# Kernel tuning notes

Hardware: AMD Instinct MI355X
Metric: run time of the kernel (lower is better)

## Reference

```python
import jax, jax.numpy as jnp
import numpy as np

IMG, P, INC = 384, 2, 3
C = 2 * IMG            # embed_dim = 768
NP_ = IMG // P         # 192 patches
N = NP_ + 1            # 193 tokens with cls
L, H, E, K, B = 6, 12, 8, 2, 32
HD = C // H
EPS = 1e-5


def layer_norm(x, w, b):
    m = jnp.mean(x, -1, keepdims=True)
    v = jnp.mean((x - m) ** 2, -1, keepdims=True)
    return (x - m) * jax.lax.rsqrt(v + EPS) * w + b


def setup_inputs() -> dict:
    key = jax.random.key(0)
    ks = iter(jax.random.split(key, 32))
    nrm = lambda sh, s=0.02: jax.random.normal(next(ks), sh, jnp.float32) * s
    inp = {
        'x1': nrm((B, INC, IMG, IMG), 1.0),
        'x2': nrm((B, INC, IMG, IMG), 1.0),
        'patch_w': nrm((C, INC, IMG, P)),
        'patch_b': jnp.zeros((C,)),
        'cls_token': nrm((1, 1, C), 1e-6),
        'ln1_w': jnp.ones((L, C)), 'ln1_b': jnp.zeros((L, C)),
        'qkv_w': nrm((L, 3 * C, C)), 'qkv_b': jnp.zeros((L, 3 * C)),
        'proj_w': nrm((L, C, C)), 'proj_b': jnp.zeros((L, C)),
        'ln2_w': jnp.ones((L, C)), 'ln2_b': jnp.zeros((L, C)),
        'route_w': nrm((L, E, C)), 'route_b': jnp.zeros((L, E)),
        'rln_w': jnp.ones((L, E)), 'rln_b': jnp.zeros((L, E)),
        'expert_w': nrm((L, E, C, C)), 'expert_b': jnp.zeros((L, E, C)),
        'norm_w': jnp.ones((C,)), 'norm_b': jnp.zeros((C,)),
    }
    # fixed 1D sin-cos positional embedding (build_sincos_encoding)
    pd = C // 2
    omega = jnp.exp(jnp.arange(pd, dtype=jnp.float32) * (-np.log(10000.0) / pd))
    ow = jnp.arange(NP_, dtype=jnp.float32)[:, None] * omega
    pe = jnp.concatenate([jnp.sin(ow), jnp.cos(ow)], axis=1)          # [192, C]
    inp['pos_emb'] = jnp.concatenate([jnp.zeros((1, C)), pe], axis=0)[None]  # [1, N, C]
    return inp


def _patch_embed(x, patch_w, patch_b, cls_token, pos_emb):
    b = x.shape[0]
    # non-overlapping (IMG, P) conv == matmul on patches, flattened in (c, kh, kw) order
    xp = x.reshape(b, INC, IMG, NP_, P).transpose(0, 3, 1, 2, 4).reshape(b, NP_, INC * IMG * P)
    tok = xp @ patch_w.reshape(C, -1).T + patch_b                     # [B, 192, C]
    tok = jnp.concatenate([jnp.broadcast_to(cls_token, (b, 1, C)), tok], axis=1)
    return tok + pos_emb


def _encoder(x, view_id, ln1_w, ln1_b, qkv_w, qkv_b, proj_w, proj_b,
             ln2_w, ln2_b, route_w, route_b, rln_w, rln_b, expert_w, expert_b):
    scale = HD ** -0.5
    base = jax.random.fold_in(jax.random.key(1234), view_id)
    b = x.shape[0]

    def step(h, p):
        idx, l1w, l1b, qw, qb, pw, pb, l2w, l2b, rw, rb, rlw, rlb, ew, eb = p
        # --- attention ---
        y = layer_norm(h, l1w, l1b)
        qkv = (y @ qw.T + qb).reshape(b, N, 3, H, HD).transpose(2, 0, 3, 1, 4)
        q, k, v = qkv[0], qkv[1], qkv[2]
        a = jax.nn.softmax(jnp.einsum('bhqd,bhkd->bhqk', q, k) * scale, axis=-1)
        o = jnp.einsum('bhqk,bhkd->bhqd', a, v).transpose(0, 2, 1, 3).reshape(b, N, C)
        h = h + o @ pw.T + pb
        # --- MoE ---
        y = layer_norm(h, l2w, l2b)
        logits = layer_norm(y @ rw.T + rb, rlw, rlb)                  # [B, N, E]
        noise = jax.random.normal(jax.random.fold_in(base, idx), logits.shape) / E
        rwts = jax.nn.softmax(logits, axis=-1) + noise
        topw, topi = jax.lax.top_k(rwts, K)
        topw = jax.nn.softmax(topw, axis=-1)
        # dense all-expert compute, as in the source module
        eo = jnp.einsum('bni,eoi->bneo', y, ew) + eb                  # [B, N, E, C]
        sel = jnp.take_along_axis(eo, topi[..., None], axis=2)        # [B, N, K, C]
        h = h + (sel * topw[..., None]).sum(axis=2)
        return h, None

    xs = (jnp.arange(L), ln1_w, ln1_b, qkv_w, qkv_b, proj_w, proj_b,
          ln2_w, ln2_b, route_w, route_b, rln_w, rln_b, expert_w, expert_b)
    x, _ = jax.lax.scan(step, x, xs)
    return x


def reference(x1, x2, patch_w, patch_b, cls_token, ln1_w, ln1_b, qkv_w, qkv_b,
              proj_w, proj_b, ln2_w, ln2_b, route_w, route_b, rln_w, rln_b,
              expert_w, expert_b, norm_w, norm_b, pos_emb):
    def tower(x, vid):
        h = _patch_embed(x, patch_w, patch_b, cls_token, pos_emb)
        h = _encoder(h, vid, ln1_w, ln1_b, qkv_w, qkv_b, proj_w, proj_b,
                     ln2_w, ln2_b, route_w, route_b, rln_w, rln_b, expert_w, expert_b)
        return layer_norm(h, norm_w, norm_b)[:, 0]
    return jnp.concatenate([tower(x1, 0), tower(x2, 1)], axis=1)      # [B, 2*C]
```

## Files before the change

kernel.cpp:

```cpp
#include <hip/hip_runtime.h>
#include <stdint.h>

#define C_DIM   768
#define N_TOK   193
#define B_TOT   64
#define ROWS    (B_TOT * N_TOK)
#define QKV_DIM 2304
#define N_HEAD  12
#define N_EXP   8
#define MAXPER  ROWS
#define RTOK    64

enum { MODE_PATCH = 0, MODE_PLAIN = 1, MODE_RESID = 2, MODE_EXPERT = 3 };

typedef __attribute__((ext_vector_type(8))) short bf16x8;
typedef __attribute__((ext_vector_type(4))) float f32x4;

__device__ __forceinline__ uint32_t rotl32(uint32_t x, int n){ return (x << n) | (x >> (32 - n)); }

__device__ __forceinline__ void tf2x32(uint32_t k0, uint32_t k1, uint32_t x0, uint32_t x1,
                                       uint32_t &r0, uint32_t &r1){
  uint32_t k2 = k0 ^ k1 ^ 0x1BD11BDAu;
#define TF4(a,b,c,d) x0+=x1; x1=rotl32(x1,a); x1^=x0; x0+=x1; x1=rotl32(x1,b); x1^=x0; \
                     x0+=x1; x1=rotl32(x1,c); x1^=x0; x0+=x1; x1=rotl32(x1,d); x1^=x0;
  x0 += k0; x1 += k1;
  TF4(13,15,26, 6)  x0 += k1; x1 += k2 + 1u;
  TF4(17,29,16,24)  x0 += k2; x1 += k0 + 2u;
  TF4(13,15,26, 6)  x0 += k0; x1 += k1 + 3u;
  TF4(17,29,16,24)  x0 += k1; x1 += k2 + 4u;
  TF4(13,15,26, 6)  x0 += k2; x1 += k0 + 5u;
#undef TF4
  r0 = x0; r1 = x1;
}

__device__ __forceinline__ float jax_erfinv(float x){
  float w = -log1pf(-x * x);
  float p;
  if (w < 5.0f){
    w -= 2.5f;
    p =              2.81022636e-08f;
    p = fmaf(p, w,   3.43273939e-07f);
    p = fmaf(p, w,  -3.5233877e-06f);
    p = fmaf(p, w,  -4.39150654e-06f);
    p = fmaf(p, w,   0.00021858087f);
    p = fmaf(p, w,  -0.00125372503f);
    p = fmaf(p, w,  -0.00417768164f);
    p = fmaf(p, w,   0.246640727f);
    p = fmaf(p, w,   1.50140941f);
  } else {
// ... 13 lines not shown

__device__ __forceinline__ float jax_noise(uint32_t c0, uint32_t c1, uint32_t j){
  uint32_t o0, o1;
  tf2x32(c0, c1, 0u, j, o0, o1);
  uint32_t bits = o0 ^ o1;
  float f = __uint_as_float(0x3f800000u | (bits >> 9)) - 1.0f;
  const float lo = -0.99999994f;
  float u = fmaxf(lo, f * 2.0f + lo);
  return 1.41421356237f * jax_erfinv(u) * 0.125f;
}

__device__ __forceinline__ unsigned short f2bf(float x){
  union { float f; uint32_t u; } v; v.f = x;
  uint32_t u = v.u;
  uint32_t r = (u + 0x7FFFu + ((u >> 16) & 1u)) >> 16;
  return (unsigned short)r;
}
__device__ __forceinline__ float bf2f(unsigned short h){
  union { uint32_t u; float f; } v; v.u = ((uint32_t)h) << 16;
  return v.f;
}
__device__ __forceinline__ void fsplit_t(float x, short &hi, short &lo){
  union { float f; uint32_t u; } v; v.f = x;
  uint32_t hb = v.u & 0xFFFF0000u;
  hi = (short)(hb >> 16);
  union { uint32_t u; float f; } hv; hv.u = hb;
  lo = (short)f2bf(x - hv.f);
}

__global__ __launch_bounds__(64) void k_sentinel(float* __restrict__ out, float v){
  if (threadIdx.x == 0) out[0] = v;
}

__global__ __launch_bounds__(256) void k_cls(float* __restrict__ h, const float* __restrict__ cls,
                                             const float* __restrict__ pos){
  const int bt = blockIdx.x;
  #pragma unroll
  for (int u = 0; u < 3; ++u){
    int c = threadIdx.x + u * 256;
    h[(size_t)bt * N_TOK * C_DIM + c] = cls[c] + pos[c];
  }
}

__device__ __forceinline__ float blk_sum(float v, float* sb){
  #pragma unroll
  for (int off = 32; off > 0; off >>= 1) v += __shfl_down(v, off, 64);
  const int lane = threadIdx.x & 63, w = threadIdx.x >> 6;
  if (lane == 0) sb[w] = v;
  __syncthreads();
  if (threadIdx.x == 0) sb[4] = sb[0] + sb[1] + sb[2] + sb[3];
  __syncthreads();
  float r = sb[4];
  __syncthreads();
  return r;
}

__global__ __launch_bounds__(256) void k_layernorm(const float* __restrict__ x, float* __restrict__ y,
                                                   const float* __restrict__ w, const float* __restrict__ b,
                                                   int* __restrict__ ecnt){
  __shared__ float sb[8];
  if (ecnt && blockIdx.x == 0 && threadIdx.x < N_EXP) ecnt[threadIdx.x] = 0;
  const float* xr = x + (size_t)blockIdx.x * C_DIM;
  float v0 = xr[threadIdx.x], v1 = xr[threadIdx.x + 256], v2 = xr[threadIdx.x + 512];
  float mean = blk_sum(v0 + v1 + v2, sb) * (1.0f / 768.0f);
  float d0 = v0 - mean, d1 = v1 - mean, d2 = v2 - mean;
  float var = blk_sum(d0 * d0 + d1 * d1 + d2 * d2, sb) * (1.0f / 768.0f);
  float inv = 1.0f / sqrtf(var + 1e-5f);
  float* yr = y + (size_t)blockIdx.x * C_DIM;
  yr[threadIdx.x]       = d0 * inv * w[threadIdx.x]       + b[threadIdx.x];
  yr[threadIdx.x + 256] = d1 * inv * w[threadIdx.x + 256] + b[threadIdx.x + 256];
  yr[threadIdx.x + 512] = d2 * inv * w[threadIdx.x + 512] + b[threadIdx.x + 512];
}

__global__ __launch_bounds__(256) void k_combine_ln(
    float* __restrict__ h, const float* __restrict__ eout, const float* __restrict__ topw,
    float* __restrict__ y, const float* __restrict__ w, const float* __restrict__ b)
{
  __shared__ float sb[8];
  const int tok = blockIdx.x;
  const float w0 = topw[tok * 2], w1 = topw[tok * 2 + 1];
  const size_t hb = (size_t)tok * C_DIM;
  const size_t e0 = (size_t)(tok * 2) * C_DIM, e1 = e0 + C_DIM;
  const int t = threadIdx.x;
  float v0 = h[hb + t]       + (w0 * eout[e0 + t]       + w1 * eout[e1 + t]);
  float v1 = h[hb + t + 256] + (w0 * eout[e0 + t + 256] + w1 * eout[e1 + t + 256]);
  float v2 = h[hb + t + 512] + (w0 * eout[e0 + t + 512] + w1 * eout[e1 + t + 512]);
  h[hb + t]       = v0;
  h[hb + t + 256] = v1;
  h[hb + t + 512] = v2;
  float mean = blk_sum(v0 + v1 + v2, sb) * (1.0f / 768.0f);
  float d0 = v0 - mean, d1 = v1 - mean, d2 = v2 - mean;
  float var = blk_sum(d0 * d0 + d1 * d1 + d2 * d2, sb) * (1.0f / 768.0f);
  float inv = 1.0f / sqrtf(var + 1e-5f);
  y[hb + t]       = d0 * inv * w[t]       + b[t];
  y[hb + t + 256] = d1 * inv * w[t + 256] + b[t + 256];
  y[hb + t + 512] = d2 * inv * w[t + 512] + b[t + 512];
}

__global__ __launch_bounds__(256) void k_final(const float* __restrict__ h, float* __restrict__ out,
                                               const float* __restrict__ w, const float* __restrict__ b){
  __shared__ float sb[8];
  const int bt = blockIdx.x;
  const float* xr = h + (size_t)bt * N_TOK * C_DIM;
  float v0 = xr[threadIdx.x], v1 = xr[threadIdx.x + 256], v2 = xr[threadIdx.x + 512];
  float mean = blk_sum(v0 + v1 + v2, sb) * (1.0f / 768.0f);
  float d0 = v0 - mean, d1 = v1 - mean, d2 = v2 - mean;
  float var = blk_sum(d0 * d0 + d1 * d1 + d2 * d2, sb) * (1.0f / 768.0f);
  float inv = 1.0f / sqrtf(var + 1e-5f);
  float* orow = out + (size_t)(bt & 31) * 1536 + (size_t)(bt >> 5) * C_DIM;
  orow[threadIdx.x]       = d0 * inv * w[threadIdx.x]       + b[threadIdx.x];
  orow[threadIdx.x + 256] = d1 * inv * w[threadIdx.x + 256] + b[threadIdx.x + 256];
  orow[threadIdx.x + 512] = d2 * inv * w[threadIdx.x + 512] + b[threadIdx.x + 512];
}

template<int MODE>
__global__ __launch_bounds__(256) void k_mgemm(
    const float* __restrict__ A, const float* __restrict__ W,
    const float* __restrict__ bias, float* __restrict__ C,
    int M, int Nc, int Kc,
    const float* __restrict__ xa, const float* __restrict__ xb,
    const float* __restrict__ pos,
    const int* __restrict__ elist, const int* __restrict__ ecnt)
{
  __shared__ short sAhi[128][40];
  __shared__ short sAlo[128][40];
  __shared__ short sBhi[128][40];
  __shared__ short sBlo[128][40];

  const int tid = threadIdx.x;

  int e = 0;
  int Mloc = M;
  const float* Wp = W;
  const float* bp = bias;
  if constexpr (MODE == MODE_EXPERT){
    e = blockIdx.z;
    Mloc = ecnt[e];
    Wp = W + (size_t)e * C_DIM * C_DIM;
    bp = bias + e * C_DIM;
  }
  const int row0 = blockIdx.x * 128;
  const int col0 = blockIdx.y * 128;
  if (row0 >= Mloc) return;

  const int srow = tid >> 1;
  const int skh  = (tid & 1) * 16;

  const float* arow = A;
  bool avalid = false;
  const float* psrc = nullptr;
  if constexpr (MODE == MODE_PLAIN || MODE == MODE_RESID){
    int r = row0 + srow;
    avalid = r < Mloc;
    arow = A + (size_t)(avalid ? r : 0) * Kc;
  } else if constexpr (MODE == MODE_EXPERT){
    int r = row0 + srow;
    avalid = r < Mloc;
    if (avalid) arow = A + (size_t)(elist[e * MAXPER + r] >> 1) * C_DIM;
  } else {
    int r = row0 + srow;
    int bt = r / 192;
    int n  = r - bt * 192;
    const float* xp = (bt < 32) ? xa : xb;
    psrc = xp + (size_t)(bt & 31) * 3 * 384 * 384 + n * 2;
    avalid = true;
  }
  const float* brow = Wp + (size_t)(col0 + srow) * Kc;

  const int wv = tid >> 6;
  const int wr = (wv >> 1) * 64;
  const int wc = (wv & 1) * 64;
  const int lane = tid & 63;
  const int lrow = lane & 15;
  const int lkh  = (lane >> 4) * 8;

  f32x4 acc[4][4] = {};

  float va[16], vb[16];
  auto loadA = [&](int k0){
    if constexpr (MODE == MODE_PATCH){
      int c   = k0 / 768;
      int rem = k0 - c * 768;
      const float* pc = psrc + ((size_t)c * 384 + (rem >> 1)) * 384;
      #pragma unroll
      for (int m = 0; m < 8; ++m){
        va[m * 2 + 0] = pc[(size_t)m * 384 + 0];
        va[m * 2 + 1] = pc[(size_t)m * 384 + 1];
      }
    } else {
      if (avalid){
        *(float4*)&va[0]  = *(const float4*)(arow + k0);
        *(float4*)&va[4]  = *(const float4*)(arow + k0 + 4);
        *(float4*)&va[8]  = *(const float4*)(arow + k0 + 8);
        *(float4*)&va[12] = *(const float4*)(arow + k0 + 12);
      } else {
        #pragma unroll
        for (int j = 0; j < 16; ++j) va[j] = 0.f;
      }
    }
  };
  auto loadB = [&](int k0){
    *(float4*)&vb[0]  = *(const float4*)(brow + k0);
    *(float4*)&vb[4]  = *(const float4*)(brow + k0 + 4);
    *(float4*)&vb[8]  = *(const float4*)(brow + k0 + 8);
    *(float4*)&vb[12] = *(const float4*)(brow + k0 + 12);
  };

  loadA(skh);
  loadB(skh);

  const int nkt = Kc / 32;
  for (int kt = 0; kt < nkt; ++kt){
    {
      short hi[16], lo[16];
      #pragma unroll
      for (int j = 0; j < 16; ++j) fsplit_t(va[j], hi[j], lo[j]);
      *(bf16x8*)&sAhi[srow][skh]     = *(bf16x8*)&hi[0];
      *(bf16x8*)&sAhi[srow][skh + 8] = *(bf16x8*)&hi[8];
      *(bf16x8*)&sAlo[srow][skh]     = *(bf16x8*)&lo[0];
      *(bf16x8*)&sAlo[srow][skh + 8] = *(bf16x8*)&lo[8];
      #pragma unroll
      for (int j = 0; j < 16; ++j) fsplit_t(vb[j], hi[j], lo[j]);
      *(bf16x8*)&sBhi[srow][skh]     = *(bf16x8*)&hi[0];
      *(bf16x8*)&sBhi[srow][skh + 8] = *(bf16x8*)&hi[8];
      *(bf16x8*)&sBlo[srow][skh]     = *(bf16x8*)&lo[0];
      *(bf16x8*)&sBlo[srow][skh + 8] = *(bf16x8*)&lo[8];
    }
    __syncthreads();
    if (kt + 1 < nkt){
      loadA((kt + 1) * 32 + skh);
      loadB((kt + 1) * 32 + skh);
    }
    bf16x8 ahi[4], alo[4], bhi[4], blo[4];
    #pragma unroll
    for (int i = 0; i < 4; ++i){
      ahi[i] = *(const bf16x8*)&sAhi[wr + i * 16 + lrow][lkh];
      alo[i] = *(const bf16x8*)&sAlo[wr + i * 16 + lrow][lkh];
    }
    #pragma unroll
    for (int j = 0; j < 4; ++j){
      bhi[j] = *(const bf16x8*)&sBhi[wc + j * 16 + lrow][lkh];
      blo[j] = *(const bf16x8*)&sBlo[wc + j * 16 + lrow][lkh];
    }
    #pragma unroll
    for (int i = 0; i < 4; ++i)
      #pragma unroll
      for (int j = 0; j < 4; ++j){
        acc[i][j] = __builtin_amdgcn_mfma_f32_16x16x32_bf16(ahi[i], bhi[j], acc[i][j], 0, 0, 0);
        acc[i][j] = __builtin_amdgcn_mfma_f32_16x16x32_bf16(ahi[i], blo[j], acc[i][j], 0, 0, 0);
        acc[i][j] = __builtin_amdgcn_mfma_f32_16x16x32_bf16(alo[i], bhi[j], acc[i][j], 0, 0, 0);
      }
    __syncthreads();
  }

  #pragma unroll
  for (int i = 0; i < 4; ++i){
    const int rbase = row0 + wr + i * 16 + (lane >> 4) * 4;
    #pragma unroll
    for (int r = 0; r < 4; ++r){
      const int rg = rbase + r;
      if (rg >= Mloc) continue;
      if constexpr (MODE == MODE_PATCH){
        int bt = rg / 192, n = rg - (rg / 192) * 192;
        size_t orow = ((size_t)bt * N_TOK + n + 1) * C_DIM;
        size_t prow = (size_t)(n + 1) * C_DIM;
        #pragma unroll
        for (int j = 0; j < 4; ++j){
          int cg = col0 + wc + j * 16 + (lane & 15);
          C[orow + cg] = acc[i][j][r] + bp[cg] + pos[prow + cg];
        }
      } else if constexpr (MODE == MODE_PLAIN){
        size_t orow = (size_t)rg * Nc;
        #pragma unroll
        for (int j = 0; j < 4; ++j){
          int cg = col0 + wc + j * 16 + (lane & 15);
          C[orow + cg] = acc[i][j][r] + bp[cg];
        }
      } else if constexpr (MODE == MODE_RESID){
        size_t orow = (size_t)rg * Nc;
        #pragma unroll
        for (int j = 0; j < 4; ++j){
          int cg = col0 + wc + j * 16 + (lane & 15);
          C[orow + cg] += acc[i][j][r] + bp[cg];
        }
      } else {
        int ts = elist[e * MAXPER + rg];
        size_t orow = (size_t)ts * C_DIM;
        #pragma unroll
        for (int j = 0; j < 4; ++j){
          int cg = col0 + wc + j * 16 + (lane & 15);
          C[orow + cg] = acc[i][j][r] + bp[cg];
        }
      }
    }
  }
}

__global__ __launch_bounds__(256) void k_attn(const float* __restrict__ qkv, float* __restrict__ o_out){
  __shared__ short sQhi[64][72],  sQlo[64][72];
  __shared__ short sKPhi[64][72], sKPlo[64][72];
  __shared__ short sVThi[64][72], sVTlo[64][72];

  const int q0 = blockIdx.x * 64;
  const int bh = blockIdx.y;
  const int bt = bh / N_HEAD, hh = bh - bt * N_HEAD;
  const int tid = threadIdx.x;
  const size_t base = (size_t)bt * N_TOK * QKV_DIM + (size_t)hh * 64;

  const int srow = tid >> 2;
  const int sk   = (tid & 3) * 16;

  {
    int q = q0 + srow;
    if (q < N_TOK){
      float v[16];
      const float* src = qkv + base + (size_t)q * QKV_DIM + sk;
      *(float4*)&v[0]  = *(const float4*)(src);
      *(float4*)&v[4]  = *(const float4*)(src + 4);
      *(float4*)&v[8]  = *(const float4*)(src + 8);
      *(float4*)&v[12] = *(const float4*)(src + 12);
      short hi[16], lo[16];
      #pragma unroll
      for (int j = 0; j < 16; ++j){
        unsigned short hb = f2bf(v[j]);
        hi[j] = (short)hb;
        lo[j] = (short)f2bf(v[j] - bf2f(hb));
      }
      *(bf16x8*)&sQhi[srow][sk]     = *(bf16x8*)&hi[0];
      *(bf16x8*)&sQhi[srow][sk + 8] = *(bf16x8*)&hi[8];
      *(bf16x8*)&sQlo[srow][sk]     = *(bf16x8*)&lo[0];
      *(bf16x8*)&sQlo[srow][sk + 8] = *(bf16x8*)&lo[8];
    } else {
      bf16x8 z = {0,0,0,0,0,0,0,0};
      *(bf16x8*)&sQhi[srow][sk]     = z;
      *(bf16x8*)&sQhi[srow][sk + 8] = z;
      *(bf16x8*)&sQlo[srow][sk]     = z;
      *(bf16x8*)&sQlo[srow][sk + 8] = z;
    }
  }

  const int wv   = tid >> 6;
  const int lane = tid & 63;
  const int lrow = lane & 15;
  const int lkh  = (lane >> 4) * 8;
  const bool wactive = (q0 + wv * 16) < N_TOK;

  f32x4 Oacc[4] = {};
  float mrun[4] = {-1e30f, -1e30f, -1e30f, -1e30f};
  float lrun[4] = {};

  for (int kt = 0; kt < 4; ++kt){
    const int n0 = kt * 64;
    __syncthreads();
    {
      int kk = n0 + srow;
      bool valid = kk < N_TOK;
      if (valid){
        float v[16];
        const float* src = qkv + base + 768 + (size_t)kk * QKV_DIM + sk;
        *(float4*)&v[0]  = *(const float4*)(src);
        *(float4*)&v[4]  = *(const float4*)(src + 4);
        *(float4*)&v[8]  = *(const float4*)(src + 8);
        *(float4*)&v[12] = *(const float4*)(src + 12);
        short hi[16], lo[16];
        #pragma unroll
        for (int j = 0; j < 16; ++j){
          unsigned short hb = f2bf(v[j]);
          hi[j] = (short)hb;
          lo[j] = (short)f2bf(v[j] - bf2f(hb));
        }
        *(bf16x8*)&sKPhi[srow][sk]     = *(bf16x8*)&hi[0];
        *(bf16x8*)&sKPhi[srow][sk + 8] = *(bf16x8*)&hi[8];
        *(bf16x8*)&sKPlo[srow][sk]     = *(bf16x8*)&lo[0];
        *(bf16x8*)&sKPlo[srow][sk + 8] = *(bf16x8*)&lo[8];
        float vv[16];
        const float* srcv = qkv + base + 1536 + (size_t)kk * QKV_DIM + sk;
        *(float4*)&vv[0]  = *(const float4*)(srcv);
        *(float4*)&vv[4]  = *(const float4*)(srcv + 4);
        *(float4*)&vv[8]  = *(const float4*)(srcv + 8);
        *(float4*)&vv[12] = *(const float4*)(srcv + 12);
        #pragma unroll
        for (int j = 0; j < 16; ++j){
          unsigned short hb = f2bf(vv[j]);
          sVThi[sk + j][srow] = (short)hb;
          sVTlo[sk + j][srow] = (short)f2bf(vv[j] - bf2f(hb));
        }
      } else {
        bf16x8 z = {0,0,0,0,0,0,0,0};
        *(bf16x8*)&sKPhi[srow][sk]     = z;
        *(bf16x8*)&sKPhi[srow][sk + 8] = z;
        *(bf16x8*)&sKPlo[srow][sk]     = z;
        *(bf16x8*)&sKPlo[srow][sk + 8] = z;
        #pragma unroll
        for (int j = 0; j < 16; ++j){
          sVThi[sk + j][srow] = 0;
          sVTlo[sk + j][srow] = 0;
        }
      }
    }
    __syncthreads();

    float p[4][4], fac[4];
    if (wactive){
      f32x4 s[4] = {};
      {
        bf16x8 ahi0 = *(const bf16x8*)&sQhi[wv * 16 + lrow][lkh];
        bf16x8 alo0 = *(const bf16x8*)&sQlo[wv * 16 + lrow][lkh];
        bf16x8 ahi1 = *(const bf16x8*)&sQhi[wv * 16 + lrow][32 + lkh];
        bf16x8 alo1 = *(const bf16x8*)&sQlo[wv * 16 + lrow][32 + lkh];
        #pragma unroll
        for (int j = 0; j < 4; ++j){
          if (n0 + j * 16 >= N_TOK) continue;
          bf16x8 bhi0 = *(const bf16x8*)&sKPhi[j * 16 + lrow][lkh];
          bf16x8 blo0 = *(const bf16x8*)&sKPlo[j * 16 + lrow][lkh];
          bf16x8 bhi1 = *(const bf16x8*)&sKPhi[j * 16 + lrow][32 + lkh];
          bf16x8 blo1 = *(const bf16x8*)&sKPlo[j * 16 + lrow][32 + lkh];
          s[j] = __builtin_amdgcn_mfma_f32_16x16x32_bf16(ahi0, bhi0, s[j], 0, 0, 0);
          s[j] = __builtin_amdgcn_mfma_f32_16x16x32_bf16(ahi0, blo0, s[j], 0, 0, 0);
          s[j] = __builtin_amdgcn_mfma_f32_16x16x32_bf16(alo0, bhi0, s[j], 0, 0, 0);
          s[j] = __builtin_amdgcn_mfma_f32_16x16x32_bf16(ahi1, bhi1, s[j], 0, 0, 0);
          s[j] = __builtin_amdgcn_mfma_f32_16x16x32_bf16(ahi1, blo1, s[j], 0, 0, 0);
          s[j] = __builtin_amdgcn_mfma_f32_16x16x32_bf16(alo1, bhi1, s[j], 0, 0, 0);
        }
      }
      #pragma unroll
      for (int j = 0; j < 4; ++j){
        bool masked = (n0 + j * 16 + lrow) >= N_TOK;
        #pragma unroll
        for (int r = 0; r < 4; ++r){
          s[j][r] *= 0.125f;
          if (masked) s[j][r] = -1e30f;
        }
      }

      #pragma unroll
      for (int r = 0; r < 4; ++r){
        float rm = fmaxf(fmaxf(s[0][r], s[1][r]), fmaxf(s[2][r], s[3][r]));
        rm = fmaxf(rm, __shfl_xor(rm, 1, 64));
        rm = fmaxf(rm, __shfl_xor(rm, 2, 64));
        rm = fmaxf(rm, __shfl_xor(rm, 4, 64));
        rm = fmaxf(rm, __shfl_xor(rm, 8, 64));
        float mn = fmaxf(mrun[r], rm);
        fac[r] = expf(mrun[r] - mn);
        mrun[r] = mn;
        lrun[r] *= fac[r];
        float rs = 0.f;
        #pragma unroll
        for (int j = 0; j < 4; ++j){ p[j][r] = expf(s[j][r] - mn); rs += p[j][r]; }
        rs += __shfl_xor(rs, 1, 64);
        rs += __shfl_xor(rs, 2, 64);
        rs += __shfl_xor(rs, 4, 64);
        rs += __shfl_xor(rs, 8, 64);
        lrun[r] += rs;
        #pragma unroll
        for (int j = 0; j < 4; ++j) Oacc[j][r] *= fac[r];
      }
    }

    __syncthreads();
    if (wactive){
      #pragma unroll
      for (int r = 0; r < 4; ++r){
        const int prow = wv * 16 + (lane >> 4) * 4 + r;
        #pragma unroll
        for (int j = 0; j < 4; ++j){
          unsigned short hb = f2bf(p[j][r]);
          sKPhi[prow][j * 16 + lrow] = (short)hb;
          sKPlo[prow][j * 16 + lrow] = (short)f2bf(p[j][r] - bf2f(hb));
        }
      }

      bf16x8 phi0 = *(const bf16x8*)&sKPhi[wv * 16 + lrow][lkh];
      bf16x8 plo0 = *(const bf16x8*)&sKPlo[wv * 16 + lrow][lkh];
      bf16x8 phi1 = *(const bf16x8*)&sKPhi[wv * 16 + lrow][32 + lkh];
      bf16x8 plo1 = *(const bf16x8*)&sKPlo[wv * 16 + lrow][32 + lkh];
      #pragma unroll
      for (int j = 0; j < 4; ++j){
        bf16x8 vhi0 = *(const bf16x8*)&sVThi[j * 16 + lrow][lkh];
        bf16x8 vlo0 = *(const bf16x8*)&sVTlo[j * 16 + lrow][lkh];
        bf16x8 vhi1 = *(const bf16x8*)&sVThi[j * 16 + lrow][32 + lkh];
        bf16x8 vlo1 = *(const bf16x8*)&sVTlo[j * 16 + lrow][32 + lkh];
        Oacc[j] = __builtin_amdgcn_mfma_f32_16x16x32_bf16(phi0, vhi0, Oacc[j], 0, 0, 0);
        Oacc[j] = __builtin_amdgcn_mfma_f32_16x16x32_bf16(phi0, vlo0, Oacc[j], 0, 0, 0);
        Oacc[j] = __builtin_amdgcn_mfma_f32_16x16x32_bf16(plo0, vhi0, Oacc[j], 0, 0, 0);
        Oacc[j] = __builtin_amdgcn_mfma_f32_16x16x32_bf16(phi1, vhi1, Oacc[j], 0, 0, 0);
        Oacc[j] = __builtin_amdgcn_mfma_f32_16x16x32_bf16(phi1, vlo1, Oacc[j], 0, 0, 0);
        Oacc[j] = __builtin_amdgcn_mfma_f32_16x16x32_bf16(plo1, vhi1, Oacc[j], 0, 0, 0);
      }
    }
  }

  if (wactive){
    #pragma unroll
    for (int r = 0; r < 4; ++r){
      int q = q0 + wv * 16 + (lane >> 4) * 4 + r;
      if (q < N_TOK){
        float inv = 1.0f / lrun[r];
        #pragma unroll
        for (int j = 0; j < 4; ++j)
          o_out[((size_t)bt * N_TOK + q) * C_DIM + hh * 64 + j * 16 + lrow] = Oacc[j][r] * inv;
      }
    }
  }
}

__global__ __launch_bounds__(256) void k_router(
    const float* __restrict__ y, const float* __restrict__ rw, const float* __restrict__ rb,
    const float* __restrict__ rlw, const float* __restrict__ rlb,
    float* __restrict__ topw, int* __restrict__ elist, int* __restrict__ ecnt, int l)
{
  __shared__ float4 sw4[1536];
  __shared__ int lcnt[8];
  __shared__ int lbase[8];
  __shared__ int llist[8][RTOK];
  const int tid = threadIdx.x;
  const float4* rw4 = (const float4*)rw;
  #pragma unroll
  for (int u = 0; u < 6; ++u)
    sw4[tid + u * 256] = rw4[tid + u * 256];
  if (tid < 8) lcnt[tid] = 0;
  __syncthreads();

  const int wid = tid >> 6, lane = tid & 63;
  const int e = lane & 7;

  for (int t16 = 0; t16 < RTOK / 4; ++t16){
    const int tok = blockIdx.x * RTOK + wid * (RTOK / 4) + t16;
    const float4* y4 = (const float4*)(y + (size_t)tok * C_DIM);
    const float4 a0 = y4[lane], a1 = y4[64 + lane], a2 = y4[128 + lane];

    float part[8];
    #pragma unroll
    for (int ee = 0; ee < 8; ++ee){
// ... 62 lines not shown
  __syncthreads();
  #pragma unroll
  for (int ee = 0; ee < 8; ++ee){
    const int cnt = lcnt[ee];
    const int bse = lbase[ee];
    for (int i = tid; i < cnt; i += 256)
      elist[ee * MAXPER + bse + i] = llist[ee][i];
  }
}

__global__ __launch_bounds__(256) void k_combine(float* __restrict__ h, const float* __restrict__ eout,
                                                 const float* __restrict__ topw){
  const int tok = blockIdx.x;
  const float w0 = topw[tok * 2], w1 = topw[tok * 2 + 1];
  const size_t hb = (size_t)tok * C_DIM;
  const size_t e0 = (size_t)(tok * 2) * C_DIM, e1 = e0 + C_DIM;
  #pragma unroll
  for (int u = 0; u < 3; ++u){
    int c = threadIdx.x + u * 256;
    h[hb + c] += w0 * eout[e0 + c] + w1 * eout[e1 + c];
  }
}

extern "C" void kernel_launch(void* const* d_in, const int* in_sizes, int n_in,
                              void* d_out, int out_size, void* d_ws, size_t ws_size,
                              hipStream_t stream){
  float* out = (float*)d_out;

  static const int kExp[22] = {
    14155776, 14155776, 1769472, 768, 768,
    4608, 4608, 10616832, 13824, 3538944, 4608,
    4608, 4608, 36864, 48, 48, 48,
    28311552, 36864, 768, 768, 148224};
  const size_t need_f = (size_t)ROWS * C_DIM * 2 + (size_t)ROWS * QKV_DIM
                      + (size_t)ROWS * 2 + (size_t)N_EXP * MAXPER + 8;
  float bad = 0.f;
  if (n_in != 22) bad = 2.0e6f;
  else {
    for (int i = 0; i < 22; ++i)
      if (in_sizes[i] != kExp[i]){ bad = 4.0e6f + i * 1.0e4f; break; }
  }
  if (bad == 0.f && out_size != 49152) bad = 3.0e6f;
  if (bad == 0.f && ws_size < need_f * 4) bad = 1.0e6f;
  if (bad != 0.f){
    k_sentinel<<<dim3(1), 64, 0, stream>>>(out, bad);
    return;
  }

  const float* x1       = (const float*)d_in[0];
  const float* x2       = (const float*)d_in[1];
  const float* patch_w  = (const float*)d_in[2];
  const float* patch_b  = (const float*)d_in[3];
  const float* cls_tok  = (const float*)d_in[4];
  const float* ln1_w    = (const float*)d_in[5];
  const float* ln1_b    = (const float*)d_in[6];
  const float* qkv_w    = (const float*)d_in[7];
  const float* qkv_b    = (const float*)d_in[8];
  const float* proj_w   = (const float*)d_in[9];
  const float* proj_b   = (const float*)d_in[10];
  const float* ln2_w    = (const float*)d_in[11];
  const float* ln2_b    = (const float*)d_in[12];
  const float* route_w  = (const float*)d_in[13];
  const float* route_b  = (const float*)d_in[14];
  const float* rln_w    = (const float*)d_in[15];
  const float* rln_b    = (const float*)d_in[16];
  const float* expert_w = (const float*)d_in[17];
  const float* expert_b = (const float*)d_in[18];
  const float* norm_w   = (const float*)d_in[19];
  const float* norm_b   = (const float*)d_in[20];
  const float* pos_emb  = (const float*)d_in[21];

  float* ws = (float*)d_ws;
  size_t off = 0;
  float* h    = ws + off; off += (size_t)ROWS * C_DIM;
  float* y    = ws + off; off += (size_t)ROWS * C_DIM;
  float* qkv  = ws + off; off += (size_t)ROWS * QKV_DIM;
  float* eout = qkv;
  float* topw = ws + off; off += (size_t)ROWS * 2;
  int*   elist = (int*)(ws + off); off += (size_t)N_EXP * MAXPER;
  int*   ecnt  = (int*)(ws + off); off += 8;

  k_cls<<<dim3(B_TOT), 256, 0, stream>>>(h, cls_tok, pos_emb);
  k_mgemm<MODE_PATCH><<<dim3(96, 6), 256, 0, stream>>>(
      nullptr, patch_w, patch_b, h, 12288, C_DIM, 2304, x1, x2, pos_emb, nullptr, nullptr);

  k_layernorm<<<dim3(ROWS), 256, 0, stream>>>(h, y, ln1_w, ln1_b, nullptr);
  for (int l = 0; l < 6; ++l){
    k_mgemm<MODE_PLAIN><<<dim3(97, 18), 256, 0, stream>>>(
        y, qkv_w + (size_t)l * QKV_DIM * C_DIM, qkv_b + l * QKV_DIM, qkv,
        ROWS, QKV_DIM, C_DIM, nullptr, nullptr, nullptr, nullptr, nullptr);
    k_attn<<<dim3(4, B_TOT * N_HEAD), 256, 0, stream>>>(qkv, y);
    k_mgemm<MODE_RESID><<<dim3(97, 6), 256, 0, stream>>>(
        y, proj_w + (size_t)l * C_DIM * C_DIM, proj_b + l * C_DIM, h,
        ROWS, C_DIM, C_DIM, nullptr, nullptr, nullptr, nullptr, nullptr);
    k_layernorm<<<dim3(ROWS), 256, 0, stream>>>(h, y, ln2_w + l * C_DIM, ln2_b + l * C_DIM, ecnt);
    k_router<<<dim3(ROWS / RTOK), 256, 0, stream>>>(
        y, route_w + (size_t)l * N_EXP * C_DIM, route_b + l * N_EXP,
        rln_w + l * N_EXP, rln_b + l * N_EXP, topw, elist, ecnt, l);
    k_mgemm<MODE_EXPERT><<<dim3(97, 6, N_EXP), 256, 0, stream>>>(
        y, expert_w + (size_t)l * N_EXP * C_DIM * C_DIM, expert_b + (size_t)l * N_EXP * C_DIM, eout,
        ROWS, C_DIM, C_DIM, nullptr, nullptr, nullptr, elist, ecnt);
    if (l < 5){
      k_combine_ln<<<dim3(ROWS), 256, 0, stream>>>(
          h, eout, topw, y, ln1_w + (l + 1) * C_DIM, ln1_b + (l + 1) * C_DIM);
    } else {
      k_combine<<<dim3(ROWS), 256, 0, stream>>>(h, eout, topw);
    }
  }
  k_final<<<dim3(B_TOT), 256, 0, stream>>>(h, out, norm_w, norm_b);
}
```

Before: 3.645 ms.

## Pre-split weights and activations into packed bf16 hi/lo layout for GEMMs

Adds a k_wsplit pass that converts fp32 weights into an interleaved bf16 hi/lo layout once per call, when workspace allows. LayerNorm, combine and attention epilogues now write activations directly in that packed layout. The GEMMs then load ready bf16 pairs instead of fp32 values, dropping the per-tile fsplit work and halving nothing in bytes but removing ALU conversion from the main loop. The cost is extra workspace, a weight conversion pass every call, and larger packed activation/weight traffic.

```diff
diff --git a/kernel.cpp b/kernel.cpp
--- a/kernel.cpp
+++ b/kernel.cpp
@@ -11,10 +11,11 @@
 #define MAXPER  ROWS
 #define RTOK    64
 
-enum { MODE_PATCH = 0, MODE_PLAIN = 1, MODE_RESID = 2, MODE_EXPERT = 3 };
+enum { MODE_PLAIN = 1, MODE_RESID = 2, MODE_EXPERT = 3 };
 
 typedef __attribute__((ext_vector_type(8))) short bf16x8;
 typedef __attribute__((ext_vector_type(4))) float f32x4;
+
 
 __device__ __forceinline__ uint32_t rotl32(uint32_t x, int n){ return (x << n) | (x >> (32 - n)); }
 
@@ -94,6 +95,25 @@
   if (threadIdx.x == 0) out[0] = v;
 }
 
+__global__ __launch_bounds__(256) void k_wsplit(const float* __restrict__ w, short* __restrict__ o, int nchunk){
+  for (int g = blockIdx.x * 256 + threadIdx.x; g < nchunk; g += gridDim.x * 256){
+    const float* src = w + (size_t)g * 16;
+    float v[16];
+    *(float4*)&v[0]  = *(const float4*)(src);
+    *(float4*)&v[4]  = *(const float4*)(src + 4);
+    *(float4*)&v[8]  = *(const float4*)(src + 8);
+    *(float4*)&v[12] = *(const float4*)(src + 12);
+    short hi[16], lo[16];
+    #pragma unroll
+    for (int j = 0; j < 16; ++j) fsplit_t(v[j], hi[j], lo[j]);
+    short* dst = o + (size_t)g * 32;
+    *(bf16x8*)(dst)      = *(bf16x8*)&hi[0];
+    *(bf16x8*)(dst + 8)  = *(bf16x8*)&hi[8];
+    *(bf16x8*)(dst + 16) = *(bf16x8*)&lo[0];
+    *(bf16x8*)(dst + 24) = *(bf16x8*)&lo[8];
+  }
+}
+
 __global__ __launch_bounds__(256) void k_cls(float* __restrict__ h, const float* __restrict__ cls,
                                              const float* __restrict__ pos){
   const int bt = blockIdx.x;
@@ -117,7 +137,16 @@
   return r;
 }
 
-__global__ __launch_bounds__(256) void k_layernorm(const float* __restrict__ x, float* __restrict__ y,
+__device__ __forceinline__ void pk_write(short* __restrict__ ypk, size_t rowbase2, int col, float o){
+  short h_, l_;
+  fsplit_t(o, h_, l_);
+  size_t ix = rowbase2 + (size_t)(col >> 4) * 32 + (col & 15);
+  ypk[ix] = h_;
+  ypk[ix + 16] = l_;
+}
+
+__global__ __launch_bounds__(256) void k_layernorm(const float* __restrict__ x, float* __restrict__ yf,
+                                                   short* __restrict__ ypk,
                                                    const float* __restrict__ w, const float* __restrict__ b,
                                                    int* __restrict__ ecnt){
   __shared__ float sb[8];
@@ -128,15 +157,22 @@
   float d0 = v0 - mean, d1 = v1 - mean, d2 = v2 - mean;
   float var = blk_sum(d0 * d0 + d1 * d1 + d2 * d2, sb) * (1.0f / 768.0f);
   float inv = 1.0f / sqrtf(var + 1e-5f);
-  float* yr = y + (size_t)blockIdx.x * C_DIM;
-  yr[threadIdx.x]       = d0 * inv * w[threadIdx.x]       + b[threadIdx.x];
-  yr[threadIdx.x + 256] = d1 * inv * w[threadIdx.x + 256] + b[threadIdx.x + 256];
-  yr[threadIdx.x + 512] = d2 * inv * w[threadIdx.x + 512] + b[threadIdx.x + 512];
+  float o0 = d0 * inv * w[threadIdx.x]       + b[threadIdx.x];
+  float o1 = d1 * inv * w[threadIdx.x + 256] + b[threadIdx.x + 256];
+  float o2 = d2 * inv * w[threadIdx.x + 512] + b[threadIdx.x + 512];
+  if (yf){
+    float* yr = yf + (size_t)blockIdx.x * C_DIM;
+    yr[threadIdx.x] = o0; yr[threadIdx.x + 256] = o1; yr[threadIdx.x + 512] = o2;
+  }
+  const size_t pb = (size_t)blockIdx.x * C_DIM * 2;
+  pk_write(ypk, pb, threadIdx.x, o0);
+  pk_write(ypk, pb, threadIdx.x + 256, o1);
+  pk_write(ypk, pb, threadIdx.x + 512, o2);
 }
 
 __global__ __launch_bounds__(256) void k_combine_ln(
     float* __restrict__ h, const float* __restrict__ eout, const float* __restrict__ topw,
-    float* __restrict__ y, const float* __restrict__ w, const float* __restrict__ b)
+    short* __restrict__ ypk, const float* __restrict__ w, const float* __restrict__ b)
 {
   __shared__ float sb[8];
   const int tok = blockIdx.x;
@@ -154,9 +190,10 @@
   float d0 = v0 - mean, d1 = v1 - mean, d2 = v2 - mean;
   float var = blk_sum(d0 * d0 + d1 * d1 + d2 * d2, sb) * (1.0f / 768.0f);
   float inv = 1.0f / sqrtf(var + 1e-5f);
-  y[hb + t]       = d0 * inv * w[t]       + b[t];
-  y[hb + t + 256] = d1 * inv * w[t + 256] + b[t + 256];
-  y[hb + t + 512] = d2 * inv * w[t + 512] + b[t + 512];
+  const size_t pb = (size_t)tok * C_DIM * 2;
+  pk_write(ypk, pb, t,       d0 * inv * w[t]       + b[t]);
+  pk_write(ypk, pb, t + 256, d1 * inv * w[t + 256] + b[t + 256]);
+  pk_write(ypk, pb, t + 512, d2 * inv * w[t + 512] + b[t + 512]);
 }
 
 __global__ __launch_bounds__(256) void k_final(const float* __restrict__ h, float* __restrict__ out,
@@ -176,12 +213,10 @@
 }
 
 template<int MODE>
-__global__ __launch_bounds__(256) void k_mgemm(
-    const float* __restrict__ A, const float* __restrict__ W,
+__global__ __launch_bounds__(256) void k_pgemm(
+    const short* __restrict__ Apk, const short* __restrict__ Wpk,
     const float* __restrict__ bias, float* __restrict__ C,
     int M, int Nc, int Kc,
-    const float* __restrict__ xa, const float* __restrict__ xb,
-    const float* __restrict__ pos,
     const int* __restrict__ elist, const int* __restrict__ ecnt)
 {
   __shared__ short sAhi[128][40];
@@ -193,12 +228,12 @@
 
   int e = 0;
   int Mloc = M;
-  const float* Wp = W;
+  const short* Wp = Wpk;
   const float* bp = bias;
   if constexpr (MODE == MODE_EXPERT){
     e = blockIdx.z;
     Mloc = ecnt[e];
-    Wp = W + (size_t)e * C_DIM * C_DIM;
+    Wp = Wpk + (size_t)e * C_DIM * C_DIM * 2;
     bp = bias + e * C_DIM;
   }
   const int row0 = blockIdx.x * 128;
@@ -208,26 +243,18 @@
   const int srow = tid >> 1;
   const int skh  = (tid & 1) * 16;
 
-  const float* arow = A;
+  const short* arow = Apk;
   bool avalid = false;
-  const float* psrc = nullptr;
   if constexpr (MODE == MODE_PLAIN || MODE == MODE_RESID){
     int r = row0 + srow;
     avalid = r < Mloc;
-    arow = A + (size_t)(avalid ? r : 0) * Kc;
-  } else if constexpr (MODE == MODE_EXPERT){
+    arow = Apk + (size_t)(avalid ? r : 0) * 2 * Kc;
+  } else {
     int r = row0 + srow;
     avalid = r < Mloc;
-    if (avalid) arow = A + (size_t)(elist[e * MAXPER + r] >> 1) * C_DIM;
-  } else {
-    int r = row0 + srow;
-    int bt = r / 192;
-    int n  = r - bt * 192;
-    const float* xp = (bt < 32) ? xa : xb;
-    psrc = xp + (size_t)(bt & 31) * 3 * 384 * 384 + n * 2;
-    avalid = true;
-  }
-  const float* brow = Wp + (size_t)(col0 + srow) * Kc;
+    if (avalid) arow = Apk + (size_t)(elist[e * MAXPER + r] >> 1) * 2 * C_DIM;
+  }
+  const short* brow = Wp + (size_t)(col0 + srow) * 2 * Kc;
 
   const int wv = tid >> 6;
   const int wr = (wv >> 1) * 64;
@@ -238,34 +265,155 @@
 
   f32x4 acc[4][4] = {};
 
-  float va[16], vb[16];
+  bf16x8 a0, a1, a2, a3, b0, b1, b2, b3;
   auto loadA = [&](int k0){
-    if constexpr (MODE == MODE_PATCH){
-      int c   = k0 / 768;
-      int rem = k0 - c * 768;
-      const float* pc = psrc + ((size_t)c * 384 + (rem >> 1)) * 384;
-      #pragma unroll
-      for (int m = 0; m < 8; ++m){
-        va[m * 2 + 0] = pc[(size_t)m * 384 + 0];
-        va[m * 2 + 1] = pc[(size_t)m * 384 + 1];
-      }
+    if (avalid){
+      const short* p = arow + (size_t)k0 * 2;
+      a0 = *(const bf16x8*)(p);
+      a1 = *(const bf16x8*)(p + 8);
+      a2 = *(const bf16x8*)(p + 16);
+      a3 = *(const bf16x8*)(p + 24);
     } else {
-      if (avalid){
-        *(float4*)&va[0]  = *(const float4*)(arow + k0);
-        *(float4*)&va[4]  = *(const float4*)(arow + k0 + 4);
-        *(float4*)&va[8]  = *(const float4*)(arow + k0 + 8);
-        *(float4*)&va[12] = *(const float4*)(arow + k0 + 12);
-      } else {
-        #pragma unroll
-        for (int j = 0; j < 16; ++j) va[j] = 0.f;
-      }
+      bf16x8 z = {0,0,0,0,0,0,0,0};
+      a0 = z; a1 = z; a2 = z; a3 = z;
     }
   };
   auto loadB = [&](int k0){
-    *(float4*)&vb[0]  = *(const float4*)(brow + k0);
-    *(float4*)&vb[4]  = *(const float4*)(brow + k0 + 4);
-    *(float4*)&vb[8]  = *(const float4*)(brow + k0 + 8);
-    *(float4*)&vb[12] = *(const float4*)(brow + k0 + 12);
+    const short* p = brow + (size_t)k0 * 2;
+    b0 = *(const bf16x8*)(p);
+    b1 = *(const bf16x8*)(p + 8);
+    b2 = *(const bf16x8*)(p + 16);
+    b3 = *(const bf16x8*)(p + 24);
+  };
+
+  loadA(skh);
+  loadB(skh);
+
+  const int nkt = Kc / 32;
+  for (int kt = 0; kt < nkt; ++kt){
+    *(bf16x8*)&sAhi[srow][skh]     = a0;
+    *(bf16x8*)&sAhi[srow][skh + 8] = a1;
+    *(bf16x8*)&sAlo[srow][skh]     = a2;
+    *(bf16x8*)&sAlo[srow][skh + 8] = a3;
+    *(bf16x8*)&sBhi[srow][skh]     = b0;
+    *(bf16x8*)&sBhi[srow][skh + 8] = b1;
+    *(bf16x8*)&sBlo[srow][skh]     = b2;
+    *(bf16x8*)&sBlo[srow][skh + 8] = b3;
+    __syncthreads();
+    if (kt + 1 < nkt){
+      loadA((kt + 1) * 32 + skh);
+      loadB((kt + 1) * 32 + skh);
+    }
+    bf16x8 ahi[4], alo[4], bhi[4], blo[4];
+    #pragma unroll
+    for (int i = 0; i < 4; ++i){
+      ahi[i] = *(const bf16x8*)&sAhi[wr + i * 16 + lrow][lkh];
+      alo[i] = *(const bf16x8*)&sAlo[wr + i * 16 + lrow][lkh];
+    }
+    #pragma unroll
+    for (int j = 0; j < 4; ++j){
+      bhi[j] = *(const bf16x8*)&sBhi[wc + j * 16 + lrow][lkh];
+      blo[j] = *(const bf16x8*)&sBlo[wc + j * 16 + lrow][lkh];
+    }
+    #pragma unroll
+    for (int i = 0; i < 4; ++i)
+      #pragma unroll
+      for (int j = 0; j < 4; ++j){
+        acc[i][j] = __builtin_amdgcn_mfma_f32_16x16x32_bf16(ahi[i], bhi[j], acc[i][j], 0, 0, 0);
+        acc[i][j] = __builtin_amdgcn_mfma_f32_16x16x32_bf16(ahi[i], blo[j], acc[i][j], 0, 0, 0);
+        acc[i][j] = __builtin_amdgcn_mfma_f32_16x16x32_bf16(alo[i], bhi[j], acc[i][j], 0, 0, 0);
+      }
+    __syncthreads();
+  }
+
+  #pragma unroll
+  for (int i = 0; i < 4; ++i){
+    const int rbase = row0 + wr + i * 16 + (lane >> 4) * 4;
+    #pragma unroll
+    for (int r = 0; r < 4; ++r){
+      const int rg = rbase + r;
+      if (rg >= Mloc) continue;
+      if constexpr (MODE == MODE_PLAIN){
+        size_t orow = (size_t)rg * Nc;
+        #pragma unroll
+        for (int j = 0; j < 4; ++j){
+          int cg = col0 + wc + j * 16 + (lane & 15);
+          C[orow + cg] = acc[i][j][r] + bp[cg];
+        }
+      } else if constexpr (MODE == MODE_RESID){
+        size_t orow = (size_t)rg * Nc;
+        #pragma unroll
+        for (int j = 0; j < 4; ++j){
+          int cg = col0 + wc + j * 16 + (lane & 15);
+          C[orow + cg] += acc[i][j][r] + bp[cg];
+        }
+      } else {
+        int ts = elist[e * MAXPER + rg];
+        size_t orow = (size_t)ts * C_DIM;
+        #pragma unroll
+        for (int j = 0; j < 4; ++j){
+          int cg = col0 + wc + j * 16 + (lane & 15);
+          C[orow + cg] = acc[i][j][r] + bp[cg];
+        }
+      }
+    }
+  }
+}
+
+__global__ __launch_bounds__(256) void k_mgemm_patch(
+    const short* __restrict__ Wpk, const float* __restrict__ bias, float* __restrict__ C,
+    const float* __restrict__ xa, const float* __restrict__ xb, const float* __restrict__ pos)
+{
+  __shared__ short sAhi[128][40];
+  __shared__ short sAlo[128][40];
+  __shared__ short sBhi[128][40];
+  __shared__ short sBlo[128][40];
+
+  const int tid = threadIdx.x;
+  const int Kc = 2304;
+  const int row0 = blockIdx.x * 128;
+  const int col0 = blockIdx.y * 128;
+
+  const int srow = tid >> 1;
+  const int skh  = (tid & 1) * 16;
+
+  const float* psrc;
+  {
+    int r = row0 + srow;
+    int bt = r / 192;
+    int n  = r - bt * 192;
+    const float* xp = (bt < 32) ? xa : xb;
+    psrc = xp + (size_t)(bt & 31) * 3 * 384 * 384 + n * 2;
+  }
+  const short* brow = Wpk + (size_t)(col0 + srow) * 2 * Kc;
+
+  const int wv = tid >> 6;
+  const int wr = (wv >> 1) * 64;
+  const int wc = (wv & 1) * 64;
+  const int lane = tid & 63;
+  const int lrow = lane & 15;
+  const int lkh  = (lane >> 4) * 8;
+
+  f32x4 acc[4][4] = {};
+
+  float va[16];
+  bf16x8 b0, b1, b2, b3;
+  auto loadA = [&](int k0){
+    int c   = k0 / 768;
+    int rem = k0 - c * 768;
+    const float* pc = psrc + ((size_t)c * 384 + (rem >> 1)) * 384;
+    #pragma unroll
+    for (int m = 0; m < 8; ++m){
+      va[m * 2 + 0] = pc[(size_t)m * 384 + 0];
+      va[m * 2 + 1] = pc[(size_t)m * 384 + 1];
+    }
+  };
+  auto loadB = [&](int k0){
+    const short* p = brow + (size_t)k0 * 2;
+    b0 = *(const bf16x8*)(p);
+    b1 = *(const bf16x8*)(p + 8);
+    b2 = *(const bf16x8*)(p + 16);
+    b3 = *(const bf16x8*)(p + 24);
   };
 
   loadA(skh);
@@ -281,12 +429,10 @@
       *(bf16x8*)&sAhi[srow][skh + 8] = *(bf16x8*)&hi[8];
       *(bf16x8*)&sAlo[srow][skh]     = *(bf16x8*)&lo[0];
       *(bf16x8*)&sAlo[srow][skh + 8] = *(bf16x8*)&lo[8];
-      #pragma unroll
-      for (int j = 0; j < 16; ++j) fsplit_t(vb[j], hi[j], lo[j]);
-      *(bf16x8*)&sBhi[srow][skh]     = *(bf16x8*)&hi[0];
-      *(bf16x8*)&sBhi[srow][skh + 8] = *(bf16x8*)&hi[8];
-      *(bf16x8*)&sBlo[srow][skh]     = *(bf16x8*)&lo[0];
-      *(bf16x8*)&sBlo[srow][skh + 8] = *(bf16x8*)&lo[8];
+      *(bf16x8*)&sBhi[srow][skh]     = b0;
+      *(bf16x8*)&sBhi[srow][skh + 8] = b1;
+      *(bf16x8*)&sBlo[srow][skh]     = b2;
+      *(bf16x8*)&sBlo[srow][skh + 8] = b3;
     }
     __syncthreads();
     if (kt + 1 < nkt){
@@ -321,44 +467,19 @@
     #pragma unroll
     for (int r = 0; r < 4; ++r){
       const int rg = rbase + r;
-      if (rg >= Mloc) continue;
-      if constexpr (MODE == MODE_PATCH){
-        int bt = rg / 192, n = rg - (rg / 192) * 192;
-        size_t orow = ((size_t)bt * N_TOK + n + 1) * C_DIM;
-        size_t prow = (size_t)(n + 1) * C_DIM;
-        #pragma unroll
-        for (int j = 0; j < 4; ++j){
-          int cg = col0 + wc + j * 16 + (lane & 15);
-          C[orow + cg] = acc[i][j][r] + bp[cg] + pos[prow + cg];
-        }
-      } else if constexpr (MODE == MODE_PLAIN){
-        size_t orow = (size_t)rg * Nc;
-        #pragma unroll
-        for (int j = 0; j < 4; ++j){
-          int cg = col0 + wc + j * 16 + (lane & 15);
-          C[orow + cg] = acc[i][j][r] + bp[cg];
-        }
-      } else if constexpr (MODE == MODE_RESID){
-        size_t orow = (size_t)rg * Nc;
-        #pragma unroll
-        for (int j = 0; j < 4; ++j){
-          int cg = col0 + wc + j * 16 + (lane & 15);
-          C[orow + cg] += acc[i][j][r] + bp[cg];
-        }
-      } else {
-        int ts = elist[e * MAXPER + rg];
-        size_t orow = (size_t)ts * C_DIM;
-        #pragma unroll
-        for (int j = 0; j < 4; ++j){
-          int cg = col0 + wc + j * 16 + (lane & 15);
-          C[orow + cg] = acc[i][j][r] + bp[cg];
-        }
-      }
-    }
-  }
-}
-
-__global__ __launch_bounds__(256) void k_attn(const float* __restrict__ qkv, float* __restrict__ o_out){
+      int bt = rg / 192, n = rg - (rg / 192) * 192;
+      size_t orow = ((size_t)bt * N_TOK + n + 1) * C_DIM;
+      size_t prow = (size_t)(n + 1) * C_DIM;
+      #pragma unroll
+      for (int j = 0; j < 4; ++j){
+        int cg = col0 + wc + j * 16 + (lane & 15);
+        C[orow + cg] = acc[i][j][r] + bias[cg] + pos[prow + cg];
+      }
+    }
+  }
+}
+
+__global__ __launch_bounds__(256) void k_attn(const float* __restrict__ qkv, short* __restrict__ opk){
   __shared__ short sQhi[64][72],  sQlo[64][72];
   __shared__ short sKPhi[64][72], sKPlo[64][72];
   __shared__ short sVThi[64][72], sVTlo[64][72];
@@ -383,11 +504,7 @@
       *(float4*)&v[12] = *(const float4*)(src + 12);
       short hi[16], lo[16];
       #pragma unroll
-      for (int j = 0; j < 16; ++j){
-        unsigned short hb = f2bf(v[j]);
-        hi[j] = (short)hb;
-        lo[j] = (short)f2bf(v[j] - bf2f(hb));
-      }
+      for (int j = 0; j < 16; ++j) fsplit_t(v[j], hi[j], lo[j]);
       *(bf16x8*)&sQhi[srow][sk]     = *(bf16x8*)&hi[0];
       *(bf16x8*)&sQhi[srow][sk + 8] = *(bf16x8*)&hi[8];
       *(bf16x8*)&sQlo[srow][sk]     = *(bf16x8*)&lo[0];
@@ -426,11 +543,7 @@
         *(float4*)&v[12] = *(const float4*)(src + 12);
         short hi[16], lo[16];
         #pragma unroll
-        for (int j = 0; j < 16; ++j){
-          unsigned short hb = f2bf(v[j]);
-          hi[j] = (short)hb;
-          lo[j] = (short)f2bf(v[j] - bf2f(hb));
-        }
+        for (int j = 0; j < 16; ++j) fsplit_t(v[j], hi[j], lo[j]);
         *(bf16x8*)&sKPhi[srow][sk]     = *(bf16x8*)&hi[0];
         *(bf16x8*)&sKPhi[srow][sk + 8] = *(bf16x8*)&hi[8];
         *(bf16x8*)&sKPlo[srow][sk]     = *(bf16x8*)&lo[0];
@@ -443,9 +556,10 @@
         *(float4*)&vv[12] = *(const float4*)(srcv + 12);
         #pragma unroll
         for (int j = 0; j < 16; ++j){
-          unsigned short hb = f2bf(vv[j]);
-          sVThi[sk + j][srow] = (short)hb;
-          sVTlo[sk + j][srow] = (short)f2bf(vv[j] - bf2f(hb));
+          short h2, l2;
+          fsplit_t(vv[j], h2, l2);
+          sVThi[sk + j][srow] = h2;
+          sVTlo[sk + j][srow] = l2;
         }
       } else {
         bf16x8 z = {0,0,0,0,0,0,0,0};
@@ -494,7 +608,6 @@
           if (masked) s[j][r] = -1e30f;
         }
       }
-
       #pragma unroll
       for (int r = 0; r < 4; ++r){
         float rm = fmaxf(fmaxf(s[0][r], s[1][r]), fmaxf(s[2][r], s[3][r]));
@@ -526,12 +639,12 @@
         const int prow = wv * 16 + (lane >> 4) * 4 + r;
         #pragma unroll
         for (int j = 0; j < 4; ++j){
-          unsigned short hb = f2bf(p[j][r]);
-          sKPhi[prow][j * 16 + lrow] = (short)hb;
-          sKPlo[prow][j * 16 + lrow] = (short)f2bf(p[j][r] - bf2f(hb));
+          short h2, l2;
+          fsplit_t(p[j][r], h2, l2);
+          sKPhi[prow][j * 16 + lrow] = h2;
+          sKPlo[prow][j * 16 + lrow] = l2;
         }
       }
-
       bf16x8 phi0 = *(const bf16x8*)&sKPhi[wv * 16 + lrow][lkh];
       bf16x8 plo0 = *(const bf16x8*)&sKPlo[wv * 16 + lrow][lkh];
       bf16x8 phi1 = *(const bf16x8*)&sKPhi[wv * 16 + lrow][32 + lkh];
@@ -558,9 +671,16 @@
       int q = q0 + wv * 16 + (lane >> 4) * 4 + r;
       if (q < N_TOK){
         float inv = 1.0f / lrun[r];
-        #pragma unroll
-        for (int j = 0; j < 4; ++j)
-          o_out[((size_t)bt * N_TOK + q) * C_DIM + hh * 64 + j * 16 + lrow] = Oacc[j][r] * inv;
+        size_t rowb = ((size_t)bt * N_TOK + q) * C_DIM * 2;
+        #pragma unroll
+        for (int j = 0; j < 4; ++j){
+          float val = Oacc[j][r] * inv;
+          short h2, l2;
+          fsplit_t(val, h2, l2);
+          size_t ix = rowb + (size_t)(hh * 4 + j) * 32 + lrow;
+          opk[ix] = h2;
+          opk[ix + 16] = l2;
+        }
       }
     }
   }
@@ -689,8 +809,15 @@
     4608, 4608, 10616832, 13824, 3538944, 4608,
     4608, 4608, 36864, 48, 48, 48,
     28311552, 36864, 768, 768, 148224};
-  const size_t need_f = (size_t)ROWS * C_DIM * 2 + (size_t)ROWS * QKV_DIM
+  const size_t W_PATCH = 1769472, W_QKV = 10616832, W_PROJ = 3538944, W_EXP = 28311552;
+  const size_t F_BASE = (size_t)ROWS * C_DIM * 2 + (size_t)ROWS * QKV_DIM
                       + (size_t)ROWS * 2 + (size_t)N_EXP * MAXPER + 8;
+  const size_t F_YPK  = (size_t)ROWS * C_DIM;
+  const size_t F_WSMALL = (size_t)N_EXP * C_DIM * C_DIM;
+  const size_t F_WFULL  = W_PATCH + W_QKV + W_PROJ + W_EXP;
+  const size_t need_small = F_BASE + F_YPK + F_WSMALL;
+  const size_t need_full  = F_BASE + F_YPK + F_WFULL;
+
   float bad = 0.f;
   if (n_in != 22) bad = 2.0e6f;
   else {
@@ -698,11 +825,12 @@
       if (in_sizes[i] != kExp[i]){ bad = 4.0e6f + i * 1.0e4f; break; }
   }
   if (bad == 0.f && out_size != 49152) bad = 3.0e6f;
-  if (bad == 0.f && ws_size < need_f * 4) bad = 1.0e6f;
+  if (bad == 0.f && ws_size < need_small * 4) bad = 1.0e6f;
   if (bad != 0.f){
     k_sentinel<<<dim3(1), 64, 0, stream>>>(out, bad);
     return;
   }
+  const bool full = ws_size >= need_full * 4;
 
   const float* x1       = (const float*)d_in[0];
   const float* x2       = (const float*)d_in[1];
@@ -736,30 +864,50 @@
   float* topw = ws + off; off += (size_t)ROWS * 2;
   int*   elist = (int*)(ws + off); off += (size_t)N_EXP * MAXPER;
   int*   ecnt  = (int*)(ws + off); off += 8;
+  short* ypk  = (short*)(ws + off); off += F_YPK;
+  short* wpk0 = (short*)(ws + off);
+
+  short *pk_patch, *pk_qkv, *pk_proj, *pk_exp;
+  if (full){
+    pk_patch = wpk0;
+    pk_qkv   = pk_patch + W_PATCH * 2;
+    pk_proj  = pk_qkv   + W_QKV * 2;
+    pk_exp   = pk_proj  + W_PROJ * 2;
+    k_wsplit<<<dim3(1024), 256, 0, stream>>>(patch_w,  pk_patch, (int)(W_PATCH / 16));
+    k_wsplit<<<dim3(2048), 256, 0, stream>>>(qkv_w,    pk_qkv,   (int)(W_QKV / 16));
+    k_wsplit<<<dim3(1024), 256, 0, stream>>>(proj_w,   pk_proj,  (int)(W_PROJ / 16));
+    k_wsplit<<<dim3(2048), 256, 0, stream>>>(expert_w, pk_exp,   (int)(W_EXP / 16));
+  } else {
+    pk_patch = pk_qkv = pk_proj = pk_exp = wpk0;
+    k_wsplit<<<dim3(1024), 256, 0, stream>>>(patch_w, wpk0, (int)(W_PATCH / 16));
+  }
 
   k_cls<<<dim3(B_TOT), 256, 0, stream>>>(h, cls_tok, pos_emb);
-  k_mgemm<MODE_PATCH><<<dim3(96, 6), 256, 0, stream>>>(
-      nullptr, patch_w, patch_b, h, 12288, C_DIM, 2304, x1, x2, pos_emb, nullptr, nullptr);
-
-  k_layernorm<<<dim3(ROWS), 256, 0, stream>>>(h, y, ln1_w, ln1_b, nullptr);
+  k_mgemm_patch<<<dim3(96, 6), 256, 0, stream>>>(pk_patch, patch_b, h, x1, x2, pos_emb);
+
+  k_layernorm<<<dim3(ROWS), 256, 0, stream>>>(h, nullptr, ypk, ln1_w, ln1_b, nullptr);
   for (int l = 0; l < 6; ++l){
-    k_mgemm<MODE_PLAIN><<<dim3(97, 18), 256, 0, stream>>>(
-        y, qkv_w + (size_t)l * QKV_DIM * C_DIM, qkv_b + l * QKV_DIM, qkv,
-        ROWS, QKV_DIM, C_DIM, nullptr, nullptr, nullptr, nullptr, nullptr);
-    k_attn<<<dim3(4, B_TOT * N_HEAD), 256, 0, stream>>>(qkv, y);
-    k_mgemm<MODE_RESID><<<dim3(97, 6), 256, 0, stream>>>(
-        y, proj_w + (size_t)l * C_DIM * C_DIM, proj_b + l * C_DIM, h,
-        ROWS, C_DIM, C_DIM, nullptr, nullptr, nullptr, nullptr, nullptr);
-    k_layernorm<<<dim3(ROWS), 256, 0, stream>>>(h, y, ln2_w + l * C_DIM, ln2_b + l * C_DIM, ecnt);
+    const size_t LQ = (size_t)QKV_DIM * C_DIM, LP = (size_t)C_DIM * C_DIM, LE = (size_t)N_EXP * C_DIM * C_DIM;
+    const short* wq = full ? pk_qkv + (size_t)l * LQ * 2 : wpk0;
+    if (!full) k_wsplit<<<dim3(1024), 256, 0, stream>>>(qkv_w + (size_t)l * LQ, wpk0, (int)(LQ / 16));
+    k_pgemm<MODE_PLAIN><<<dim3(97, 18), 256, 0, stream>>>(
+        ypk, wq, qkv_b + l * QKV_DIM, qkv, ROWS, QKV_DIM, C_DIM, nullptr, nullptr);
+    k_attn<<<dim3(4, B_TOT * N_HEAD), 256, 0, stream>>>(qkv, ypk);
+    const short* wp = full ? pk_proj + (size_t)l * LP * 2 : wpk0;
+    if (!full) k_wsplit<<<dim3(512), 256, 0, stream>>>(proj_w + (size_t)l * LP, wpk0, (int)(LP / 16));
+    k_pgemm<MODE_RESID><<<dim3(97, 6), 256, 0, stream>>>(
+        ypk, wp, proj_b + l * C_DIM, h, ROWS, C_DIM, C_DIM, nullptr, nullptr);
+    k_layernorm<<<dim3(ROWS), 256, 0, stream>>>(h, y, ypk, ln2_w + l * C_DIM, ln2_b + l * C_DIM, ecnt);
     k_router<<<dim3(ROWS / RTOK), 256, 0, stream>>>(
         y, route_w + (size_t)l * N_EXP * C_DIM, route_b + l * N_EXP,
         rln_w + l * N_EXP, rln_b + l * N_EXP, topw, elist, ecnt, l);
-    k_mgemm<MODE_EXPERT><<<dim3(97, 6, N_EXP), 256, 0, stream>>>(
-        y, expert_w + (size_t)l * N_EXP * C_DIM * C_DIM, expert_b + (size_t)l * N_EXP * C_DIM, eout,
-        ROWS, C_DIM, C_DIM, nullptr, nullptr, nullptr, elist, ecnt);
+    const short* we = full ? pk_exp + (size_t)l * LE * 2 : wpk0;
+    if (!full) k_wsplit<<<dim3(2048), 256, 0, stream>>>(expert_w + (size_t)l * LE, wpk0, (int)(LE / 16));
+    k_pgemm<MODE_EXPERT><<<dim3(97, 6, N_EXP), 256, 0, stream>>>(
+        ypk, we, expert_b + (size_t)l * N_EXP * C_DIM, eout, ROWS, C_DIM, C_DIM, elist, ecnt);
     if (l < 5){
       k_combine_ln<<<dim3(ROWS), 256, 0, stream>>>(
-          h, eout, topw, y, ln1_w + (l + 1) * C_DIM, ln1_b + (l + 1) * C_DIM);
+          h, eout, topw, ypk, ln1_w + (l + 1) * C_DIM, ln1_b + (l + 1) * C_DIM);
     } else {
       k_combine<<<dim3(ROWS), 256, 0, stream>>>(h, eout, topw);
     }
```

Result: slower. 4.156 ms (+14.0%).
